# Performance work log

Hardware: AMD Instinct MI355X
Metric: run time of the kernel (lower is better)

The kernel has to match this reference:

```python
import jax, jax.numpy as jnp
import numpy as np

N = 50000   # nodes
E = 600000  # edges
D = 128     # in = hidden = out channels
G = 256     # graphs in batch
EPS = 1e-5


def setup_inputs() -> dict:
    key = jax.random.key(0)
    ks = jax.random.split(key, 16)
    sc = 1.0 / np.sqrt(D)
    inp = {
        "x": jax.random.normal(ks[0], (N, D), jnp.float32),
        "edge_index": jax.random.randint(ks[1], (2, E), 0, N, dtype=jnp.int32),
        "edge_attr": jax.random.normal(ks[2], (E, 4), jnp.float32),
        "batch": jnp.sort(jax.random.randint(ks[3], (N,), 0, G, dtype=jnp.int32)),
        # conv1 + norm1
        "W1": jax.random.normal(ks[4], (D, D), jnp.float32) * sc,
        "b1": jnp.zeros((D,), jnp.float32),
        "g1": jnp.ones((D,), jnp.float32),
        "be1": jnp.zeros((D,), jnp.float32),
        # middle conv (num_layers=3 -> one hidden conv) + norm
        "Wm": jax.random.normal(ks[5], (D, D), jnp.float32) * sc,
        "bm": jnp.zeros((D,), jnp.float32),
        "gm": jnp.ones((D,), jnp.float32),
        "bem": jnp.zeros((D,), jnp.float32),
        # conv2 + norm2
        "W2": jax.random.normal(ks[6], (D, D), jnp.float32) * sc,
        "b2": jnp.zeros((D,), jnp.float32),
        "g2": jnp.ones((D,), jnp.float32),
        "be2": jnp.zeros((D,), jnp.float32),
    }
    return inp


def _gcn_conv(x, W, b, src, dst, dinv):
    # PyG GCNConv with add_self_loops=True: out = D^{-1/2}(A+I)D^{-1/2} (x W) + b
    h = x @ W
    enorm = dinv[src] * dinv[dst]                      # [E]
    msg = h[src] * enorm[:, None]                      # gather + scale
    agg = jnp.zeros_like(h).at[dst].add(msg)           # scatter-add to targets
    agg = agg + h * (dinv * dinv)[:, None]             # self-loop contribution
    return agg + b


def _bn(x, g, b):
    # BatchNorm1d over nodes (batch statistics)
    mu = jnp.mean(x, axis=0)
    var = jnp.var(x, axis=0)
    return (x - mu) * jax.lax.rsqrt(var + EPS) * g + b


def reference(x, edge_index, edge_attr, batch,
              W1, b1, g1, be1, Wm, bm, gm, bem, W2, b2, g2, be2):
    src, dst = edge_index[0], edge_index[1]
    # degree of A + I (in-degree at targets, +1 self loop); shared by all layers
    deg = jnp.zeros((N,), x.dtype).at[dst].add(1.0) + 1.0
    dinv = jax.lax.rsqrt(deg)

    h = jax.nn.relu(_bn(_gcn_conv(x, W1, b1, src, dst, dinv), g1, be1))
    h = jax.nn.relu(_bn(_gcn_conv(h, Wm, bm, src, dst, dinv), gm, bem))
    h = _bn(_gcn_conv(h, W2, b2, src, dst, dinv), g2, be2)

    # global mean pool (batch re-based at batch[0])
    seg = batch - batch[0]
    sums = jax.ops.segment_sum(h, seg, num_segments=G)
    cnt = jax.ops.segment_sum(jnp.ones((N,), h.dtype), seg, num_segments=G)
    return sums / jnp.maximum(cnt, 1.0)[:, None]
```

## Files before the change

kernel.cpp:

```cpp
#include <hip/hip_runtime.h>

#define DIM 128
constexpr float EPS = 1e-5f;
#define SHARD 2048

typedef _Float16 f16;
typedef __attribute__((ext_vector_type(8))) _Float16 f16x8;
typedef __attribute__((ext_vector_type(4))) float f32x4;

__global__ __launch_bounds__(256) void k_prep(const int* __restrict__ dst,
                                              int* __restrict__ degi, int E,
                                              const float* __restrict__ W0,
                                              const float* __restrict__ W1,
                                              const float* __restrict__ W2,
                                              f16* __restrict__ wt) {
    if (blockIdx.x < 12) {
        int layer = blockIdx.x >> 2;
        int quarter = blockIdx.x & 3;
        const float* W = layer == 0 ? W0 : (layer == 1 ? W1 : W2);
        f16* hi = wt + (size_t)layer * 2 * DIM * DIM;
        f16* lo = hi + DIM * DIM;
        for (int idx = quarter * 4096 + threadIdx.x; idx < (quarter + 1) * 4096;
             idx += 256) {
            int k = idx >> 7, c = idx & 127;
            float w = W[idx];
            f16 h = (f16)w;
            f16 l = (f16)((w - (float)h) * 2048.0f);
            hi[c * DIM + k] = h;
            lo[c * DIM + k] = l;
        }
    } else {
        int e = (blockIdx.x - 12) * 256 + threadIdx.x;
        if (e < E) atomicAdd(&degi[dst[e]], 1);
    }
}

__global__ __launch_bounds__(256) void k_scan_local(const int* __restrict__ degi,
                                                    int* __restrict__ row_ptr,
                                                    float* __restrict__ dinv,
                                                    int* __restrict__ bsum, int n) {
    __shared__ int ws[4];
    int t = threadIdx.x, lane = t & 63, wv = t >> 6;
    int i0 = blockIdx.x * 1024 + t * 4;
    int v[4];
#pragma unroll
    for (int j = 0; j < 4; ++j) {
        int i = i0 + j;
        v[j] = (i < n) ? degi[i] : 0;
        if (i < n) dinv[i] = rsqrtf((float)v[j] + 1.0f);
    }
    int tsum = v[0] + v[1] + v[2] + v[3];
    int sc = tsum;
#pragma unroll
    for (int off = 1; off < 64; off <<= 1) {
        int u = __shfl_up(sc, off, 64);
        if (lane >= off) sc += u;
    }
    if (lane == 63) ws[wv] = sc;
    __syncthreads();
    int woff = 0;
    for (int j = 0; j < wv; ++j) woff += ws[j];
    int run = woff + sc - tsum;
#pragma unroll
    for (int j = 0; j < 4; ++j) {
        int i = i0 + j;
        if (i < n) row_ptr[i] = run;
        run += v[j];
    }
    if (t == 255) bsum[blockIdx.x] = woff + sc;
}

__global__ __launch_bounds__(256) void k_scan_add(int* __restrict__ row_ptr,
                                                  int* __restrict__ cursor,
                                                  const int* __restrict__ bsum,
                                                  int n, int E, int nb) {
    __shared__ int soff;
    int t = threadIdx.x;
    int seg = blockIdx.x >> 2;
    if (t < 64) {
        int v = (t < nb) ? bsum[t] : 0;
        int sc = v;
#pragma unroll
        for (int off = 1; off < 64; off <<= 1) {
            int u = __shfl_up(sc, off, 64);
            if (t >= off) sc += u;
        }
        if (t == seg) soff = sc - v;
    }
    __syncthreads();
    int i = blockIdx.x * 256 + t;
    if (i < n) {
        int v = row_ptr[i] + soff;
        row_ptr[i] = v;
        cursor[i] = v;
    }
    if (i == 0) row_ptr[n] = E;
}

__global__ void k_fill(const int* __restrict__ src, const int* __restrict__ dst,
                       int* __restrict__ cursor, int* __restrict__ csr_src, int E) {
    int e = blockIdx.x * blockDim.x + threadIdx.x;
    if (e >= E) return;
    int d = dst[e];
    int slot = atomicAdd(&cursor[d], 1);
    csr_src[slot] = src[e];
}

template <bool PRE_BN>
__global__ __launch_bounds__(256) void k_matmul_mfma(
    const float* __restrict__ inF, const f16* __restrict__ inH,
    const f16* __restrict__ wt, const float* __restrict__ dinv,
    const float* __restrict__ stats, const float* __restrict__ g,
    const float* __restrict__ be, float inv_n, f16* __restrict__ out, int n) {
    __shared__ __align__(16) char sA[64 * 256];
    __shared__ float sScale[DIM], sShift[DIM];

    int t = threadIdx.x;
    int w = t >> 6, l = t & 63;
    int row0 = blockIdx.x * 64;

    if (PRE_BN) {
        if (t < DIM) {
            float su = 0.f, sq = 0.f;
#pragma unroll
            for (int s = 0; s < 8; ++s) {
                su += stats[s * 256 + t];
                sq += stats[s * 256 + 128 + t];
            }
            float mu = su * inv_n;
            float var = sq * inv_n - mu * mu;
            float sc = rsqrtf(var + EPS) * g[t];
            sScale[t] = sc;
            sShift[t] = be[t] - mu * sc;
        }
        __syncthreads();
    }

    f16x8 bh[2][4], bl[2][4];
    {
        int col = w * 32 + (l & 15);
        int ksub = (l >> 4) * 8;
        const f16* hi = wt;
        const f16* lo = wt + DIM * DIM;
#pragma unroll
        for (int ct = 0; ct < 2; ++ct) {
            int c2 = col + ct * 16;
#pragma unroll
            for (int kt = 0; kt < 4; ++kt) {
                bh[ct][kt] = *(const f16x8*)&hi[(size_t)c2 * DIM + kt * 32 + ksub];
                bl[ct][kt] = *(const f16x8*)&lo[(size_t)c2 * DIM + kt * 32 + ksub];
            }
        }
    }

    {
        int r = t >> 2;
        int row_g = row0 + r;
        if (row_g >= n) row_g = n - 1;
        int cbase = (t & 3) * 32;
#pragma unroll
        for (int o = 0; o < 4; ++o) {
            int c0 = cbase + o * 8;
            f16x8 h8;
            if (PRE_BN) {
                f16x8 v8 = *(const f16x8*)(inH + (size_t)row_g * DIM + c0);
#pragma unroll
                for (int j = 0; j < 8; ++j) {
                    float v = (float)v8[j] * sScale[c0 + j] + sShift[c0 + j];
                    h8[j] = (f16)fmaxf(v, 0.f);
                }
            } else {
                float4 v0 = *(const float4*)(inF + (size_t)row_g * DIM + c0);
                float4 v1 = *(const float4*)(inF + (size_t)row_g * DIM + c0 + 4);
                h8[0] = (f16)v0.x; h8[1] = (f16)v0.y; h8[2] = (f16)v0.z; h8[3] = (f16)v0.w;
                h8[4] = (f16)v1.x; h8[5] = (f16)v1.y; h8[6] = (f16)v1.z; h8[7] = (f16)v1.w;
            }
            int byte = (r * 256 + c0 * 2) ^ ((r & 7) << 4);
            *(f16x8*)(sA + byte) = h8;
        }
    }
    __syncthreads();

    f32x4 accA[4][2], accB[4][2];
#pragma unroll
    for (int rt = 0; rt < 4; ++rt)
#pragma unroll
        for (int ct = 0; ct < 2; ++ct) {
            accA[rt][ct] = (f32x4){0.f, 0.f, 0.f, 0.f};
            accB[rt][ct] = (f32x4){0.f, 0.f, 0.f, 0.f};
        }

#pragma unroll
    for (int rt = 0; rt < 4; ++rt) {
        int row_l = rt * 16 + (l & 15);
        int kb = (l >> 4) * 16;
        f16x8 a[4];
#pragma unroll
        for (int kt = 0; kt < 4; ++kt) {
            int byte = (row_l * 256 + kt * 64 + kb) ^ ((row_l & 7) << 4);
            a[kt] = *(const f16x8*)(sA + byte);
        }
#pragma unroll
        for (int ct = 0; ct < 2; ++ct) {
            f32x4 cA = accA[rt][ct], cB = accB[rt][ct];
#pragma unroll
            for (int kt = 0; kt < 4; ++kt) {
                cA = __builtin_amdgcn_mfma_f32_16x16x32_f16(a[kt], bh[ct][kt], cA, 0, 0, 0);
                cB = __builtin_amdgcn_mfma_f32_16x16x32_f16(a[kt], bl[ct][kt], cB, 0, 0, 0);
            }
            accA[rt][ct] = cA;
            accB[rt][ct] = cB;
        }
    }

    int colw = w * 32 + (l & 15);
#pragma unroll
    for (int rt = 0; rt < 4; ++rt) {
        int row_l = rt * 16 + ((l >> 4) << 2);
#pragma unroll
        for (int reg = 0; reg < 4; ++reg) {
            int gr = row0 + row_l + reg;
            if (gr >= n) continue;
            float dv = dinv[gr];
#pragma unroll
            for (int ct = 0; ct < 2; ++ct) {
                float v = (accA[rt][ct][reg] + accB[rt][ct][reg] * (1.0f / 2048.0f)) * dv;
                out[(size_t)gr * DIM + colw + ct * 16] = (f16)v;
            }
        }
    }
}

template <bool POOL>
__global__ __launch_bounds__(1024) void k_gs(const f16* __restrict__ hs,
                                             const int* __restrict__ csr_src,
                                             const int* __restrict__ row_ptr,
                                             const float* __restrict__ dinv,
                                             const float* __restrict__ b,
                                             const int* __restrict__ batch,
                                             f16* __restrict__ agg,
                                             float* __restrict__ stats_part,
                                             float* __restrict__ gsum, int n) {
    __shared__ float sSum[16][DIM];
    __shared__ float sSq[16][DIM];
    __shared__ int sSeg[16];

    int t = threadIdx.x;
    int wv = t >> 6, l = t & 63;
    int node = blockIdx.x * 16 + wv;
    int grp = l >> 4;
    int c8 = (l & 15) * 8;
    bool valid = node < n;

    float acc[8] = {};
    int beg = 0, end = 0;
    if (valid) {
        beg = row_ptr[node];
        end = row_ptr[node + 1];
    }
    int e = beg + grp;
    for (; e + 4 < end; e += 8) {
        int s0 = csr_src[e];
        int s1 = csr_src[e + 4];
        f16x8 a = *(const f16x8*)(hs + (size_t)s0 * DIM + c8);
        f16x8 c = *(const f16x8*)(hs + (size_t)s1 * DIM + c8);
#pragma unroll
        for (int j = 0; j < 8; ++j) acc[j] += (float)a[j] + (float)c[j];
    }
    for (; e < end; e += 4) {
        int s0 = csr_src[e];
        f16x8 a = *(const f16x8*)(hs + (size_t)s0 * DIM + c8);
#pragma unroll
        for (int j = 0; j < 8; ++j) acc[j] += (float)a[j];
    }
#pragma unroll
    for (int j = 0; j < 8; ++j) {
        acc[j] += __shfl_xor(acc[j], 16, 64);
        acc[j] += __shfl_xor(acc[j], 32, 64);
    }

    if (grp == 0) {
        if (valid) {
            f16x8 hv = *(const f16x8*)(hs + (size_t)node * DIM + c8);
            float dv = dinv[node];
            f32x4 bb0 = *(const f32x4*)(b + c8);
            f32x4 bb1 = *(const f32x4*)(b + c8 + 4);
            float o[8];
#pragma unroll
            for (int j = 0; j < 4; ++j) {
                o[j] = (acc[j] + (float)hv[j]) * dv + bb0[j];
                o[j + 4] = (acc[j + 4] + (float)hv[j + 4]) * dv + bb1[j];
            }
            f16x8 ov;
#pragma unroll
            for (int j = 0; j < 8; ++j) ov[j] = (f16)o[j];
            *(f16x8*)(agg + (size_t)node * DIM + c8) = ov;
            f32x4 s0 = {o[0], o[1], o[2], o[3]}, s1 = {o[4], o[5], o[6], o[7]};
            f32x4 q0 = {o[0]*o[0], o[1]*o[1], o[2]*o[2], o[3]*o[3]};
            f32x4 q1 = {o[4]*o[4], o[5]*o[5], o[6]*o[6], o[7]*o[7]};
            *(f32x4*)&sSum[wv][c8] = s0;
            *(f32x4*)&sSum[wv][c8 + 4] = s1;
            *(f32x4*)&sSq[wv][c8] = q0;
            *(f32x4*)&sSq[wv][c8 + 4] = q1;
            if (POOL && l == 0) sSeg[wv] = batch[node] - batch[0];
        } else {
            f32x4 z = {0.f, 0.f, 0.f, 0.f};
            *(f32x4*)&sSum[wv][c8] = z;
            *(f32x4*)&sSum[wv][c8 + 4] = z;
            *(f32x4*)&sSq[wv][c8] = z;
            *(f32x4*)&sSq[wv][c8 + 4] = z;
        }
    }
    __syncthreads();

    int shard = (blockIdx.x & 7) * 256;
    if (t < 128) {
        float s = 0.f;
#pragma unroll
        for (int w = 0; w < 16; ++w) s += sSum[w][t];
        atomicAdd(&stats_part[shard + t], s);
    } else if (t < 256) {
        int ch = t - 128;
        float s = 0.f;
#pragma unroll
        for (int w = 0; w < 16; ++w) s += sSq[w][ch];
        atomicAdd(&stats_part[shard + 128 + ch], s);
    }

    if (POOL && t < 128) {
        int cur = -1;
        float a = 0.f;
        for (int w = 0; w < 16; ++w) {
            if (blockIdx.x * 16 + w >= n) break;
            int seg = sSeg[w];
            if (seg != cur) {
                if (cur >= 0) atomicAdd(&gsum[(size_t)cur * DIM + t], a);
                a = 0.f;
                cur = seg;
            }
            a += sSum[w][t];
        }
        if (cur >= 0) atomicAdd(&gsum[(size_t)cur * DIM + t], a);
    }
}

__global__ __launch_bounds__(128) void k_pool_fin(const float* __restrict__ gsum,
                                                  const int* __restrict__ batch,
                                                  const float* __restrict__ stats,
                                                  const float* __restrict__ g,
                                                  const float* __restrict__ be,
                                                  float* __restrict__ out,
                                                  int n, float inv_n) {
    int gseg = blockIdx.x;
    int c = threadIdx.x;
    int b0 = batch[0];
    int target = b0 + gseg;
    int lo = 0, hi = n;
    while (lo < hi) { int mid = (lo + hi) >> 1; if (batch[mid] < target) lo = mid + 1; else hi = mid; }
    int start = lo;
    lo = start; hi = n;
    while (lo < hi) { int mid = (lo + hi) >> 1; if (batch[mid] < target + 1) lo = mid + 1; else hi = mid; }
    int end = lo;
    int cnt = end - start;

    float su = 0.f, sq = 0.f;
#pragma unroll
    for (int s = 0; s < 8; ++s) {
        su += stats[s * 256 + c];
        sq += stats[s * 256 + 128 + c];
    }
    float mu = su * inv_n;
    float var = sq * inv_n - mu * mu;
    float scale = rsqrtf(var + EPS) * g[c];
    float shift = be[c] - mu * scale;
    float o = 0.f;
    if (cnt > 0) o = (gsum[(size_t)gseg * DIM + c] / (float)cnt) * scale + shift;
    out[(size_t)gseg * DIM + c] = o;
}

extern "C" void kernel_launch(void* const* d_in, const int* in_sizes, int n_in,
                              void* d_out, int out_size, void* d_ws, size_t ws_size,
                              hipStream_t stream) {
    const float* x = (const float*)d_in[0];
    const int* edge_index = (const int*)d_in[1];
    const int* batch = (const int*)d_in[3];
    const float* W1 = (const float*)d_in[4];
    const float* b1 = (const float*)d_in[5];
    const float* g1 = (const float*)d_in[6];
    const float* be1 = (const float*)d_in[7];
    const float* Wm = (const float*)d_in[8];
    const float* bm = (const float*)d_in[9];
    const float* gm = (const float*)d_in[10];
    const float* bem = (const float*)d_in[11];
    const float* W2 = (const float*)d_in[12];
    const float* b2 = (const float*)d_in[13];
    const float* g2 = (const float*)d_in[14];
    const float* be2 = (const float*)d_in[15];

    int n = in_sizes[0] / DIM;
    int E = in_sizes[1] / 2;
    int G = out_size / DIM;

    const int* srcI = edge_index;
    const int* dstI = edge_index + E;

    char* p = (char*)d_ws;
    f16* bufA = (f16*)p;                p += (size_t)n * DIM * 2;
    f16* bufB = (f16*)p;                p += (size_t)n * DIM * 2;
    float* dinv = (float*)p;            p += (size_t)n * 4;
    int* row_ptr = (int*)p;             p += (size_t)(n + 1) * 4;
    int* cursor = (int*)p;              p += (size_t)n * 4;
    int* csr_src = (int*)p;             p += (size_t)E * 4;
    int* bsum = (int*)p;                p += 64 * 4;
    char* zero0 = p;
    int* degi = (int*)p;                p += (size_t)n * 4;
    float* stats3 = (float*)p;          p += 3 * SHARD * 4;
    float* gsum = (float*)p;            p += (size_t)G * DIM * 4;
    size_t zero_bytes = (size_t)(p - zero0);
    f16* wsplit = (f16*)p;              p += (size_t)3 * 2 * DIM * DIM * 2;

    float* out = (float*)d_out;
    float inv_n = 1.0f / (float)n;
    int nb = (n + 1023) / 1024;

    hipMemsetAsync(zero0, 0, zero_bytes, stream);
    k_prep<<<12 + (E + 255) / 256, 256, 0, stream>>>(dstI, degi, E, W1, Wm, W2, wsplit);
    k_scan_local<<<nb, 256, 0, stream>>>(degi, row_ptr, dinv, bsum, n);
    k_scan_add<<<(n + 255) / 256, 256, 0, stream>>>(row_ptr, cursor, bsum, n, E, nb);
    k_fill<<<(E + 255) / 256, 256, 0, stream>>>(srcI, dstI, cursor, csr_src, E);

    struct Layer { const float *b, *g, *be; };
    Layer L[3] = {{b1, g1, be1}, {bm, gm, bem}, {b2, g2, be2}};

    int mmBlocks = (n + 63) / 64;
    int gsBlocks = (n + 15) / 16;
    for (int l = 0; l < 3; ++l) {
        const f16* wl = wsplit + (size_t)l * 2 * DIM * DIM;
        float* stats_l = stats3 + l * SHARD;
        if (l == 0)
            k_matmul_mfma<false><<<mmBlocks, 256, 0, stream>>>(
                x, nullptr, wl, dinv, nullptr, nullptr, nullptr, inv_n, bufA, n);
        else
            k_matmul_mfma<true><<<mmBlocks, 256, 0, stream>>>(
                nullptr, bufB, wl, dinv, stats3 + (l - 1) * SHARD,
                L[l - 1].g, L[l - 1].be, inv_n, bufA, n);
        if (l < 2)
            k_gs<false><<<gsBlocks, 1024, 0, stream>>>(bufA, csr_src, row_ptr, dinv,
                                                       L[l].b, batch, bufB, stats_l,
                                                       nullptr, n);
        else
            k_gs<true><<<gsBlocks, 1024, 0, stream>>>(bufA, csr_src, row_ptr, dinv,
                                                      L[l].b, batch, bufB, stats_l,
                                                      gsum, n);
    }

    k_pool_fin<<<G, 128, 0, stream>>>(gsum, batch, stats3 + 2 * SHARD, g2, be2,
                                      out, n, inv_n);
}
```

Measured before the change: 280.8 us.

## Process multiple nodes per wave in gather-scatter kernel with register-held stats

```diff
diff --git a/kernel.cpp b/kernel.cpp
--- a/kernel.cpp
+++ b/kernel.cpp
@@ -232,59 +232,62 @@
 }
 
 template <bool POOL>
-__global__ __launch_bounds__(1024) void k_gs(const f16* __restrict__ hs,
-                                             const int* __restrict__ csr_src,
-                                             const int* __restrict__ row_ptr,
-                                             const float* __restrict__ dinv,
-                                             const float* __restrict__ b,
-                                             const int* __restrict__ batch,
-                                             f16* __restrict__ agg,
-                                             float* __restrict__ stats_part,
-                                             float* __restrict__ gsum, int n) {
-    __shared__ float sSum[16][DIM];
-    __shared__ float sSq[16][DIM];
-    __shared__ int sSeg[16];
-
-    int t = threadIdx.x;
-    int wv = t >> 6, l = t & 63;
-    int node = blockIdx.x * 16 + wv;
-    int grp = l >> 4;
-    int c8 = (l & 15) * 8;
-    bool valid = node < n;
-
-    float acc[8] = {};
-    int beg = 0, end = 0;
-    if (valid) {
-        beg = row_ptr[node];
-        end = row_ptr[node + 1];
-    }
-    int e = beg + grp;
-    for (; e + 4 < end; e += 8) {
-        int s0 = csr_src[e];
-        int s1 = csr_src[e + 4];
-        f16x8 a = *(const f16x8*)(hs + (size_t)s0 * DIM + c8);
-        f16x8 c = *(const f16x8*)(hs + (size_t)s1 * DIM + c8);
-#pragma unroll
-        for (int j = 0; j < 8; ++j) acc[j] += (float)a[j] + (float)c[j];
-    }
-    for (; e < end; e += 4) {
-        int s0 = csr_src[e];
-        f16x8 a = *(const f16x8*)(hs + (size_t)s0 * DIM + c8);
-#pragma unroll
-        for (int j = 0; j < 8; ++j) acc[j] += (float)a[j];
-    }
-#pragma unroll
-    for (int j = 0; j < 8; ++j) {
-        acc[j] += __shfl_xor(acc[j], 16, 64);
-        acc[j] += __shfl_xor(acc[j], 32, 64);
-    }
-
+__global__ __launch_bounds__(256) void k_gs(const f16* __restrict__ hs,
+                                            const int* __restrict__ csr_src,
+                                            const int* __restrict__ row_ptr,
+                                            const float* __restrict__ dinv,
+                                            const float* __restrict__ b,
+                                            const int* __restrict__ batch,
+                                            f16* __restrict__ agg,
+                                            float* __restrict__ stats_part,
+                                            float* __restrict__ gsum,
+                                            int n, int chunk) {
+    __shared__ float sred[4][256];
+    __shared__ float sPool[4][DIM];
+    __shared__ int sSegId[4];
+
+    int t = threadIdx.x, wv = t >> 6, l = t & 63;
+    int grp = l >> 4, c8 = (l & 15) * 8;
+    int wid = blockIdx.x * 4 + wv;
+    int r0 = wid * chunk;
+    int r1 = min(n, r0 + chunk);
+
+    float ssum[8] = {}, ssq[8] = {}, pacc[8] = {};
+    int curseg = -1;
+    int b0 = POOL ? batch[0] : 0;
+    f32x4 bb0 = {0,0,0,0}, bb1 = {0,0,0,0};
     if (grp == 0) {
-        if (valid) {
+        bb0 = *(const f32x4*)(b + c8);
+        bb1 = *(const f32x4*)(b + c8 + 4);
+    }
+
+    int beg = (r0 < r1) ? row_ptr[r0] : 0;
+    for (int node = r0; node < r1; ++node) {
+        int end = row_ptr[node + 1];
+        float acc[8] = {};
+        int e = beg + grp;
+        for (; e + 4 < end; e += 8) {
+            int s0 = csr_src[e];
+            int s1 = csr_src[e + 4];
+            f16x8 a = *(const f16x8*)(hs + (size_t)s0 * DIM + c8);
+            f16x8 c = *(const f16x8*)(hs + (size_t)s1 * DIM + c8);
+#pragma unroll
+            for (int j = 0; j < 8; ++j) acc[j] += (float)a[j] + (float)c[j];
+        }
+        for (; e < end; e += 4) {
+            int s0 = csr_src[e];
+            f16x8 a = *(const f16x8*)(hs + (size_t)s0 * DIM + c8);
+#pragma unroll
+            for (int j = 0; j < 8; ++j) acc[j] += (float)a[j];
+        }
+#pragma unroll
+        for (int j = 0; j < 8; ++j) {
+            acc[j] += __shfl_xor(acc[j], 16, 64);
+            acc[j] += __shfl_xor(acc[j], 32, 64);
+        }
+        if (grp == 0) {
             f16x8 hv = *(const f16x8*)(hs + (size_t)node * DIM + c8);
             float dv = dinv[node];
-            f32x4 bb0 = *(const f32x4*)(b + c8);
-            f32x4 bb1 = *(const f32x4*)(b + c8 + 4);
             float o[8];
 #pragma unroll
             for (int j = 0; j < 4; ++j) {
@@ -295,50 +298,57 @@
 #pragma unroll
             for (int j = 0; j < 8; ++j) ov[j] = (f16)o[j];
             *(f16x8*)(agg + (size_t)node * DIM + c8) = ov;
-            f32x4 s0 = {o[0], o[1], o[2], o[3]}, s1 = {o[4], o[5], o[6], o[7]};
-            f32x4 q0 = {o[0]*o[0], o[1]*o[1], o[2]*o[2], o[3]*o[3]};
-            f32x4 q1 = {o[4]*o[4], o[5]*o[5], o[6]*o[6], o[7]*o[7]};
-            *(f32x4*)&sSum[wv][c8] = s0;
-            *(f32x4*)&sSum[wv][c8 + 4] = s1;
-            *(f32x4*)&sSq[wv][c8] = q0;
-            *(f32x4*)&sSq[wv][c8 + 4] = q1;
-            if (POOL && l == 0) sSeg[wv] = batch[node] - batch[0];
-        } else {
-            f32x4 z = {0.f, 0.f, 0.f, 0.f};
-            *(f32x4*)&sSum[wv][c8] = z;
-            *(f32x4*)&sSum[wv][c8 + 4] = z;
-            *(f32x4*)&sSq[wv][c8] = z;
-            *(f32x4*)&sSq[wv][c8 + 4] = z;
+#pragma unroll
+            for (int j = 0; j < 8; ++j) {
+                ssum[j] += o[j];
+                ssq[j] += o[j] * o[j];
+            }
+            if (POOL) {
+                int seg = batch[node] - b0;
+                if (seg != curseg) {
+                    if (curseg >= 0) {
+#pragma unroll
+                        for (int j = 0; j < 8; ++j)
+                            atomicAdd(&gsum[(size_t)curseg * DIM + c8 + j], pacc[j]);
+                    }
+#pragma unroll
+                    for (int j = 0; j < 8; ++j) pacc[j] = 0.f;
+                    curseg = seg;
+                }
+#pragma unroll
+                for (int j = 0; j < 8; ++j) pacc[j] += o[j];
+            }
+        }
+        beg = end;
+    }
+
+    if (grp == 0) {
+#pragma unroll
+        for (int j = 0; j < 8; ++j) {
+            sred[wv][c8 + j] = ssum[j];
+            sred[wv][128 + c8 + j] = ssq[j];
+        }
+        if (POOL) {
+#pragma unroll
+            for (int j = 0; j < 8; ++j) sPool[wv][c8 + j] = pacc[j];
+            if (l == 0) sSegId[wv] = curseg;
         }
     }
     __syncthreads();
-
-    int shard = (blockIdx.x & 7) * 256;
-    if (t < 128) {
-        float s = 0.f;
-#pragma unroll
-        for (int w = 0; w < 16; ++w) s += sSum[w][t];
-        atomicAdd(&stats_part[shard + t], s);
-    } else if (t < 256) {
-        int ch = t - 128;
-        float s = 0.f;
-#pragma unroll
-        for (int w = 0; w < 16; ++w) s += sSq[w][ch];
-        atomicAdd(&stats_part[shard + 128 + ch], s);
-    }
-
+    float s = sred[0][t] + sred[1][t] + sred[2][t] + sred[3][t];
+    atomicAdd(&stats_part[(blockIdx.x & 7) * 256 + t], s);
     if (POOL && t < 128) {
         int cur = -1;
         float a = 0.f;
-        for (int w = 0; w < 16; ++w) {
-            if (blockIdx.x * 16 + w >= n) break;
-            int seg = sSeg[w];
-            if (seg != cur) {
+        for (int w = 0; w < 4; ++w) {
+            int sg = sSegId[w];
+            if (sg < 0) continue;
+            if (sg != cur) {
                 if (cur >= 0) atomicAdd(&gsum[(size_t)cur * DIM + t], a);
                 a = 0.f;
-                cur = seg;
-            }
-            a += sSum[w][t];
+                cur = sg;
+            }
+            a += sPool[w][t];
         }
         if (cur >= 0) atomicAdd(&gsum[(size_t)cur * DIM + t], a);
     }
@@ -433,7 +443,8 @@
     Layer L[3] = {{b1, g1, be1}, {bm, gm, bem}, {b2, g2, be2}};
 
     int mmBlocks = (n + 63) / 64;
-    int gsBlocks = (n + 15) / 16;
+    const int CHUNK = 8;
+    int gsBlocks = (n + 4 * CHUNK - 1) / (4 * CHUNK);
     for (int l = 0; l < 3; ++l) {
         const f16* wl = wsplit + (size_t)l * 2 * DIM * DIM;
         float* stats_l = stats3 + l * SHARD;
@@ -445,13 +456,13 @@
                 nullptr, bufB, wl, dinv, stats3 + (l - 1) * SHARD,
                 L[l - 1].g, L[l - 1].be, inv_n, bufA, n);
         if (l < 2)
-            k_gs<false><<<gsBlocks, 1024, 0, stream>>>(bufA, csr_src, row_ptr, dinv,
-                                                       L[l].b, batch, bufB, stats_l,
-                                                       nullptr, n);
+            k_gs<false><<<gsBlocks, 256, 0, stream>>>(bufA, csr_src, row_ptr, dinv,
+                                                      L[l].b, batch, bufB, stats_l,
+                                                      nullptr, n, CHUNK);
         else
-            k_gs<true><<<gsBlocks, 1024, 0, stream>>>(bufA, csr_src, row_ptr, dinv,
-                                                      L[l].b, batch, bufB, stats_l,
-                                                      gsum, n);
+            k_gs<true><<<gsBlocks, 256, 0, stream>>>(bufA, csr_src, row_ptr, dinv,
+                                                     L[l].b, batch, bufB, stats_l,
+                                                     gsum, n, CHUNK);
     }
 
     k_pool_fin<<<G, 128, 0, stream>>>(gsum, batch, stats3 + 2 * SHARD, g2, be2,
```

Result: no change. 285.2 us (+1.6%).
